# Kernel tuning notes

Measured on AMD Instinct MI355X. Metric: run time of the kernel, lower is better.

The kernel has to match this reference:

```python
import jax, jax.numpy as jnp
import numpy as np

V = 50257   # vocab_size
D = 128     # embed_dim
B = 1024    # batch of center words
C = 10      # context window size


def setup_inputs() -> dict:
    key = jax.random.key(0)
    ks = jax.random.split(key, 12)
    s = 0.05  # small init scale for linear weights
    return {
        "center_id": jax.random.randint(ks[0], (B,), 0, V),
        "context_ids": jax.random.randint(ks[1], (B, C), 0, V),
        "epsilon": jax.random.normal(ks[2], (D,), dtype=jnp.float32),
        # embedding tables init uniform(-1, 1) as in the torch module
        "emb": jax.random.uniform(ks[3], (V, D), minval=-1.0, maxval=1.0, dtype=jnp.float32),
        "prior_means": jax.random.uniform(ks[4], (V, D), minval=-1.0, maxval=1.0, dtype=jnp.float32),
        "prior_vars": jax.random.uniform(ks[5], (V, D), minval=-1.0, maxval=1.0, dtype=jnp.float32),
        "W_enc": jax.random.normal(ks[6], (2 * D, 2 * D), dtype=jnp.float32) * s,
        "b_enc": jnp.zeros((2 * D,), dtype=jnp.float32),
        "W_mean": jax.random.normal(ks[7], (2 * D, D), dtype=jnp.float32) * s,
        "b_mean": jnp.zeros((D,), dtype=jnp.float32),
        "W_var": jax.random.normal(ks[8], (2 * D, D), dtype=jnp.float32) * s,
        "b_var": jnp.zeros((D,), dtype=jnp.float32),
        "W_vocab": jax.random.normal(ks[9], (D, V), dtype=jnp.float32) * s,
        "b_vocab": jnp.zeros((V,), dtype=jnp.float32),
    }


def reference(center_id, context_ids, epsilon, emb, prior_means, prior_vars,
              W_enc, b_enc, W_mean, b_mean, W_var, b_var, W_vocab, b_vocab):
    ce = emb[center_id]                       # [B, D]
    cx = emb[context_ids]                     # [B, C, D]
    enc_in = jnp.concatenate(
        [jnp.broadcast_to(ce[:, None, :], cx.shape), cx], axis=-1)  # [B, C, 2D]
    h = jax.nn.relu(enc_in @ W_enc + b_enc).sum(axis=1)  # [B, 2D]
    mean = h @ W_mean + b_mean                           # [B, D]
    var = jax.nn.softplus(h @ W_var + b_var)             # [B, D] (diag cov s0)
    z = mean + jnp.exp(var / 2.0) * epsilon              # single shared epsilon [D]
    logits = z @ W_vocab + b_vocab                        # [B, V]
    logp = jax.nn.log_softmax(logits, axis=1)             # log(categorical)

    pm = prior_means[center_id]                           # m1 [B, D]
    pv = jax.nn.softplus(prior_vars[center_id])           # diag cov s1 [B, D]
    diff = pm - mean
    # closed-form diagonal Gaussian KL, identical math to the
    # trace/inverse/det formulation over diagflat matrices in the source
    kl = 0.5 * jnp.sum(var / pv + diff * diff / pv - 1.0
                       + jnp.log(pv) - jnp.log(var), axis=1)  # [B]

    # reconstruction: sum_k log categorical[i, context_ids[i, k]]
    rec = jnp.take_along_axis(logp, context_ids, axis=1).sum(axis=1)  # [B]

    return jnp.mean(rec - kl)
```

## Files before the change

### kernel.cpp

```cpp
#include <hip/hip_runtime.h>
#include <math.h>

#define VV 50257
#define VPAD 50304
#define DD 128
#define BB 1024
#define CC 10

typedef short bf16x8 __attribute__((ext_vector_type(8)));
typedef float f32x4 __attribute__((ext_vector_type(4)));

__device__ inline float bf2f(unsigned short u) {
    return __uint_as_float(((unsigned)u) << 16);
}
__device__ inline unsigned short f2bf(float f) {
    unsigned u = __float_as_uint(f);
    unsigned r = ((u >> 16) & 1) + 0x7FFF;
    return (unsigned short)((u + r) >> 16);
}


__global__ __launch_bounds__(256) void k_prep0(
    const float* __restrict__ W_enc, unsigned short* __restrict__ WeP)
{
    __shared__ float tl[256][17];
    const int jg = blockIdx.x, tid = threadIdx.x;
#pragma unroll
    for (int i = 0; i < 16; ++i) {
        int idx = i * 256 + tid;
        int k = idx >> 4, j = idx & 15;
        tl[k][j] = W_enc[(size_t)k * 256 + jg * 16 + j];
    }
    __syncthreads();
#pragma unroll
    for (int i = 0; i < 2; ++i) {
        int c = i * 256 + tid;
        int l15 = c & 15, q = (c >> 4) & 3, kI = c >> 6;
        bf16x8 o;
#pragma unroll
        for (int e = 0; e < 8; ++e)
            o[e] = (short)f2bf(tl[kI * 32 + q * 8 + e][l15]);
        *(bf16x8*)(WeP + (((size_t)jg * 8 + kI) * 64 + q * 16 + l15) * 8) = o;
    }
}

#define AS_STRIDE 520
__global__ __launch_bounds__(256) void k_main(
    const int* __restrict__ center_id, const int* __restrict__ context_ids,
    const float* __restrict__ emb, const unsigned short* __restrict__ WeP,
    const float* __restrict__ b_enc, const float* __restrict__ Wv,
    const float* __restrict__ W_mean, const float* __restrict__ W_var,
    unsigned short* __restrict__ WvP, unsigned short* __restrict__ Wmv,
    float* __restrict__ h)
{
    __shared__ __align__(16) unsigned char smraw[50688];
    const int bid = blockIdx.x, tid = threadIdx.x;

    if (bid >= 818) {
        const int b4 = bid - 818;
#pragma unroll
        for (int i = 0; i < 32; ++i) {
            int idx = b4 * 8192 + i * 256 + tid;
            unsigned short m = f2bf(W_mean[idx]);
            unsigned short v = f2bf(W_var[idx]);
            *(ushort2*)(Wmv + (size_t)idx * 2) = make_ushort2(m, v);
        }
        return;
    }

    if (bid >= 32) {
        float (*tile)[65] = (float (*)[65])smraw;
        const int s = bid - 32;
        const int v0 = s * 64;
#pragma unroll
        for (int i = 0; i < 32; ++i) {
            int idx = tid + i * 256;
            int k = idx >> 6, j = idx & 63;
            int v = v0 + j;
            tile[k][j] = (v < VV) ? Wv[(size_t)k * VV + v] : 0.f;
        }
        __syncthreads();
#pragma unroll
        for (int i = 0; i < 4; ++i) {
            int c = i * 256 + tid;
            int l15 = c & 15, q = (c >> 4) & 3, kI = (c >> 6) & 3, g = c >> 8;
            bf16x8 o;
#pragma unroll
            for (int e = 0; e < 8; ++e)
                o[e] = (short)f2bf(tile[kI * 32 + q * 8 + e][g * 16 + l15]);
            size_t vg = (size_t)s * 4 + g;
            *(bf16x8*)(WvP + ((vg * 4 + kI) * 64 + q * 16 + l15) * 8) = o;
        }
        return;
    }

    unsigned short* As = (unsigned short*)smraw;

    const int lane = tid & 63;
    const int wid  = tid >> 6;
    const int wm   = wid & 1;
    const int wn   = wid >> 1;
    const int quad = lane >> 4;
    const int l15  = lane & 15;

    const int bt = bid & 15;
    const int zt = bid >> 4;
    const int b0 = bt * 64;
    const int n0 = zt * 128;

    const int rlane = tid >> 4;
    const int c8    = tid & 15;
    const int kIc   = c8 >> 2, qc = c8 & 3;

#pragma unroll
    for (int p = 0; p < 4; ++p) {
        int r = p * 16 + rlane;
        int rid_ce = center_id[b0 + r];
        const float* s0 = emb + (size_t)rid_ce * 128 + c8 * 8;
        float4 a0 = *(const float4*)s0, a1 = *(const float4*)(s0 + 4);
        bf16x8 oa;
        oa[0] = (short)f2bf(a0.x); oa[1] = (short)f2bf(a0.y);
        oa[2] = (short)f2bf(a0.z); oa[3] = (short)f2bf(a0.w);
        oa[4] = (short)f2bf(a1.x); oa[5] = (short)f2bf(a1.y);
        oa[6] = (short)f2bf(a1.z); oa[7] = (short)f2bf(a1.w);
        *(bf16x8*)(As + (size_t)(p * 8 + kIc) * AS_STRIDE + (qc * 16 + rlane) * 8) = oa;
    }
#pragma unroll
    for (int p = 0; p < 4; ++p) {
        int r = p * 16 + rlane;
        int rid_cx = context_ids[(b0 + r) * CC + 0];
        const float* s1 = emb + (size_t)rid_cx * 128 + c8 * 8;
        float4 b0v = *(const float4*)s1, b1v = *(const float4*)(s1 + 4);
        bf16x8 ob;
        ob[0] = (short)f2bf(b0v.x); ob[1] = (short)f2bf(b0v.y);
        ob[2] = (short)f2bf(b0v.z); ob[3] = (short)f2bf(b0v.w);
        ob[4] = (short)f2bf(b1v.x); ob[5] = (short)f2bf(b1v.y);
        ob[6] = (short)f2bf(b1v.z); ob[7] = (short)f2bf(b1v.w);
        *(bf16x8*)(As + (size_t)(p * 8 + kIc + 4) * AS_STRIDE + (qc * 16 + rlane) * 8) = ob;
    }
    __syncthreads();

    float benc[4];
#pragma unroll
    for (int nt = 0; nt < 4; ++nt)
        benc[nt] = b_enc[n0 + wn * 64 + nt * 16 + l15];

    bf16x8 bbot[4][4];
#pragma unroll
    for (int nt = 0; nt < 4; ++nt) {
        size_t jg = (size_t)zt * 8 + wn * 4 + nt;
#pragma unroll
        for (int kI = 0; kI < 4; ++kI)
            bbot[nt][kI] = *(const bf16x8*)(WeP + ((jg * 8 + kI + 4) * 64 + lane) * 8);
    }

    f32x4 acc_ce[2][4];
#pragma unroll
    for (int mt = 0; mt < 2; ++mt)
#pragma unroll
        for (int nt = 0; nt < 4; ++nt) acc_ce[mt][nt] = (f32x4){0.f, 0.f, 0.f, 0.f};
#pragma unroll
    for (int kI = 0; kI < 4; ++kI) {
        bf16x8 a[2], b[4];
#pragma unroll
        for (int mt = 0; mt < 2; ++mt)
            a[mt] = *(const bf16x8*)(As + (size_t)((wm * 2 + mt) * 8 + kI) * AS_STRIDE + lane * 8);
#pragma unroll
        for (int nt = 0; nt < 4; ++nt) {
            size_t jg = (size_t)zt * 8 + wn * 4 + nt;
            b[nt] = *(const bf16x8*)(WeP + ((jg * 8 + kI) * 64 + lane) * 8);
        }
#pragma unroll
        for (int mt = 0; mt < 2; ++mt)
#pragma unroll
            for (int nt = 0; nt < 4; ++nt)
                acc_ce[mt][nt] = __builtin_amdgcn_mfma_f32_16x16x32_bf16(
                    a[mt], b[nt], acc_ce[mt][nt], 0, 0, 0);
    }

    float hacc[2][4][4];
#pragma unroll
    for (int mt = 0; mt < 2; ++mt)
#pragma unroll
        for (int nt = 0; nt < 4; ++nt)
#pragma unroll
            for (int reg = 0; reg < 4; ++reg) hacc[mt][nt][reg] = 0.f;

    for (int c = 0; c < CC; ++c) {
        f32x4 acc[2][4];
#pragma unroll
        for (int mt = 0; mt < 2; ++mt)
#pragma unroll
            for (int nt = 0; nt < 4; ++nt) acc[mt][nt] = acc_ce[mt][nt];
#pragma unroll
        for (int kI = 0; kI < 4; ++kI) {
            bf16x8 a[2];
#pragma unroll
            for (int mt = 0; mt < 2; ++mt)
                a[mt] = *(const bf16x8*)(As + (size_t)((wm * 2 + mt) * 8 + kI + 4) * AS_STRIDE + lane * 8);
#pragma unroll
            for (int mt = 0; mt < 2; ++mt)
#pragma unroll
                for (int nt = 0; nt < 4; ++nt)
                    acc[mt][nt] = __builtin_amdgcn_mfma_f32_16x16x32_bf16(
                        a[mt], bbot[nt][kI], acc[mt][nt], 0, 0, 0);
        }
#pragma unroll
        for (int mt = 0; mt < 2; ++mt)
#pragma unroll
            for (int nt = 0; nt < 4; ++nt)
#pragma unroll
                for (int reg = 0; reg < 4; ++reg)
                    hacc[mt][nt][reg] += fmaxf(acc[mt][nt][reg] + benc[nt], 0.f);

        if (c < CC - 1) {
            __syncthreads();
#pragma unroll
            for (int p = 0; p < 4; ++p) {
                int r = p * 16 + rlane;
                int rid_cx = context_ids[(b0 + r) * CC + (c + 1)];
                const float* s1 = emb + (size_t)rid_cx * 128 + c8 * 8;
                float4 b0v = *(const float4*)s1, b1v = *(const float4*)(s1 + 4);
                bf16x8 ob;
                ob[0] = (short)f2bf(b0v.x); ob[1] = (short)f2bf(b0v.y);
                ob[2] = (short)f2bf(b0v.z); ob[3] = (short)f2bf(b0v.w);
                ob[4] = (short)f2bf(b1v.x); ob[5] = (short)f2bf(b1v.y);
                ob[6] = (short)f2bf(b1v.z); ob[7] = (short)f2bf(b1v.w);
                *(bf16x8*)(As + (size_t)(p * 8 + kIc + 4) * AS_STRIDE + (qc * 16 + rlane) * 8) = ob;
            }
            __syncthreads();
        }
    }

    __syncthreads();
    float (*Csf)[132] = (float (*)[132])smraw;
#pragma unroll
    for (int mt = 0; mt < 2; ++mt)
#pragma unroll
        for (int nt = 0; nt < 4; ++nt) {
            int col = wn * 64 + nt * 16 + l15;
#pragma unroll
            for (int reg = 0; reg < 4; ++reg) {
                int row = wm * 32 + mt * 16 + quad * 4 + reg;
                Csf[row][col] = hacc[mt][nt][reg];
            }
        }
    __syncthreads();
#pragma unroll
    for (int it = 0; it < 8; ++it) {
        int ch = it * 256 + tid;
        int row = ch >> 5, cg = ch & 31;
        *(float4*)&h[(size_t)(b0 + row) * 256 + n0 + cg * 4] = *(const float4*)&Csf[row][cg * 4];
    }
}

__global__ __launch_bounds__(512) void k_latent(
    const float* __restrict__ h, const unsigned short* __restrict__ Wmv,
    const float* __restrict__ b_mean, const float* __restrict__ b_var,
    const float* __restrict__ epsilon,
    const int* __restrict__ center_id, const int* __restrict__ context_ids,
    const unsigned short* __restrict__ WvP, const float* __restrict__ bv,
    const float* __restrict__ prior_means, const float* __restrict__ prior_vars,
    unsigned short* __restrict__ z_pack, float* __restrict__ kl,
    float* __restrict__ ctxsum, float* __restrict__ out)
{
    __shared__ __align__(16) float hs[4][256];
    __shared__ float mpart[3][4][128], vpart[3][4][128];
    __shared__ float zsh[4][128];
    __shared__ float red[4][2];
    __shared__ float credw[4][2];
    const int tid = threadIdx.x;
    const int b0 = blockIdx.x * 4;

    if (blockIdx.x == 0 && tid == 0) out[0] = 0.f;

    {
        const int col = tid & 255;
        const int rr  = tid >> 8;
#pragma unroll
        for (int r2 = 0; r2 < 2; ++r2) {
            int row = rr * 2 + r2;
            hs[row][col] = h[(size_t)(b0 + row) * 256 + col];
        }
    }
    __syncthreads();

    const int d    = tid & 127;
    const int part = tid >> 7;
    const int kbase = part * 64;
    float m[4], vr[4];
#pragma unroll
    for (int r = 0; r < 4; ++r) {
        m[r]  = part ? 0.f : b_mean[d];
        vr[r] = part ? 0.f : b_var[d];
    }
    for (int k0 = 0; k0 < 64; k0 += 4) {
        float4 h4[4];
#pragma unroll
        for (int r = 0; r < 4; ++r)
            h4[r] = *(const float4*)&hs[r][kbase + k0];
#pragma unroll
        for (int kk = 0; kk < 4; ++kk) {
            ushort2 u = *(const ushort2*)(Wmv + ((size_t)(kbase + k0 + kk) * 128 + d) * 2);
            float wm_ = bf2f(u.x), wv_ = bf2f(u.y);
#pragma unroll
            for (int r = 0; r < 4; ++r) {
                float hk = ((const float*)&h4[r])[kk];
                m[r]  += hk * wm_;
                vr[r] += hk * wv_;
            }
        }
    }
    if (part) {
#pragma unroll
        for (int r = 0; r < 4; ++r) {
            mpart[part - 1][r][d] = m[r];
            vpart[part - 1][r][d] = vr[r];
        }
    }
    __syncthreads();

    if (tid < 128) {
        const int wid = tid >> 6;
        const int kIz = d >> 5, qz = (d >> 3) & 3, ez = d & 7;
        const int bg = b0 >> 4;
#pragma unroll
        for (int r = 0; r < 4; ++r) {
            float mm = m[r]  + mpart[0][r][d] + mpart[1][r][d] + mpart[2][r][d];
            float vv = vr[r] + vpart[0][r][d] + vpart[1][r][d] + vpart[2][r][d];

            float var = (vv > 20.f) ? vv : log1pf(__expf(vv));
            float zd = mm + __expf(0.5f * var) * epsilon[d];
            unsigned short zu = f2bf(zd);
            const int bb = b0 + r;
            const int l15b = bb & 15;
            z_pack[(((size_t)(bg * 4 + kIz)) * 64 + qz * 16 + l15b) * 8 + ez] = zu;
            zsh[r][d] = bf2f(zu);

            int cid = center_id[bb];
            float pm  = prior_means[(size_t)cid * 128 + d];
            float pvr = prior_vars[(size_t)cid * 128 + d];
            float pv  = (pvr > 20.f) ? pvr : log1pf(__expf(pvr));
            float diff = pm - mm;
            float t = var / pv + diff * diff / pv - 1.f + logf(pv) - logf(var);
#pragma unroll
            for (int off = 32; off; off >>= 1) t += __shfl_xor(t, off, 64);
            if ((tid & 63) == 0) red[r][wid] = t;
        }
    }
    __syncthreads();

    {
        const int w     = tid >> 6;
        const int row   = w & 3;
        const int phalf = w >> 2;
        const int lane  = tid & 63;
        const float z1 = zsh[row][lane];
        const float z2 = zsh[row][lane + 64];
        const int kI1 = lane >> 5, q1 = (lane >> 3) & 3, e1 = lane & 7;
        const int d2  = lane + 64;
        const int kI2 = d2 >> 5,  q2 = (d2 >> 3) & 3,  e2 = d2 & 7;
        float cacc = 0.f;
#pragma unroll
        for (int pp = 0; pp < 5; ++pp) {
            int p = phalf * 5 + pp;
            int cid = context_ids[(b0 + row) * CC + p];
            int vg = cid >> 4, l15v = cid & 15;
            float w1 = bf2f(WvP[(((size_t)(vg * 4 + kI1)) * 64 + q1 * 16 + l15v) * 8 + e1]);
            float w2 = bf2f(WvP[(((size_t)(vg * 4 + kI2)) * 64 + q2 * 16 + l15v) * 8 + e2]);
            float cs = z1 * w1 + z2 * w2;
#pragma unroll
            for (int off = 32; off; off >>= 1) cs += __shfl_xor(cs, off, 64);
            cacc += cs + bv[cid];
        }
        if (lane == 0) credw[row][phalf] = cacc;
    }
    __syncthreads();
    if (tid < 4) {
        kl[b0 + tid]     = 0.5f * (red[tid][0] + red[tid][1]);
        ctxsum[b0 + tid] = credw[tid][0] + credw[tid][1];
    }
}

__global__ __launch_bounds__(256) void k_lse(
    const unsigned short* __restrict__ z_pack, const unsigned short* __restrict__ WvP,
    const float* __restrict__ bv, float* __restrict__ partial)
{
    __shared__ float pl[2][128][20];
    const int x = blockIdx.x + 8 * blockIdx.y;
    if (x >= 393) return;
    const int mg = blockIdx.z;

    const int tid  = threadIdx.x;
    const int lane = tid & 63;
    const int wid  = tid >> 6;
    const int wm   = wid & 1;
    const int wn   = wid >> 1;
    const int quad = lane >> 4;
    const int l15  = lane & 15;
    const int n0   = x * 128;

    bf16x8 bfr[4][4];
#pragma unroll
    for (int nt = 0; nt < 4; ++nt) {
        size_t vg = (size_t)x * 8 + wn * 4 + nt;
#pragma unroll
        for (int kI = 0; kI < 4; ++kI)
            bfr[nt][kI] = *(const bf16x8*)(WvP + ((vg * 4 + kI) * 64 + lane) * 8);
    }

    float bvf[4];
#pragma unroll
    for (int nt = 0; nt < 4; ++nt) {
        int n = n0 + wn * 64 + nt * 16 + l15;
        bvf[nt] = (n < VV) ? bv[n] : -__builtin_huge_valf();
    }

#pragma unroll
    for (int mi = 0; mi < 4; ++mi) {
        const int mi_g = mg * 4 + mi;

        f32x4 acc[4][4];
#pragma unroll
        for (int mt = 0; mt < 4; ++mt)
#pragma unroll
            for (int nt = 0; nt < 4; ++nt) acc[mt][nt] = (f32x4){0.f, 0.f, 0.f, 0.f};

#pragma unroll
        for (int kI = 0; kI < 4; ++kI) {
            bf16x8 afr[4];
#pragma unroll
            for (int mt = 0; mt < 4; ++mt) {
                size_t bg = (size_t)mi_g * 8 + wm * 4 + mt;
                afr[mt] = *(const bf16x8*)(z_pack + ((bg * 4 + kI) * 64 + lane) * 8);
            }
#pragma unroll
            for (int mt = 0; mt < 4; ++mt)
#pragma unroll
                for (int nt = 0; nt < 4; ++nt)
                    acc[mt][nt] = __builtin_amdgcn_mfma_f32_16x16x32_bf16(
                        afr[mt], bfr[nt][kI], acc[mt][nt], 0, 0, 0);
        }

#pragma unroll
        for (int mt = 0; mt < 4; ++mt)
#pragma unroll
            for (int reg = 0; reg < 4; ++reg) {
                float s = 0.f;
#pragma unroll
                for (int nt = 0; nt < 4; ++nt)
                    s += __expf(acc[mt][nt][reg] + bvf[nt]);
                pl[wn][wm * 64 + mt * 16 + quad * 4 + reg][l15] = s;
            }
        __syncthreads();
        if (tid < 128) {
            const float* p0 = &pl[0][tid][0];
            const float* p1 = &pl[1][tid][0];
            float4 a0 = *(const float4*)(p0);
            float4 a1 = *(const float4*)(p0 + 4);
            float4 a2 = *(const float4*)(p0 + 8);
            float4 a3 = *(const float4*)(p0 + 12);
            float4 b0 = *(const float4*)(p1);
            float4 b1 = *(const float4*)(p1 + 4);
            float4 b2 = *(const float4*)(p1 + 8);
            float4 b3 = *(const float4*)(p1 + 12);
            float tot = (a0.x + a0.y + a0.z + a0.w) + (a1.x + a1.y + a1.z + a1.w)
                      + (a2.x + a2.y + a2.z + a2.w) + (a3.x + a3.y + a3.z + a3.w)
                      + (b0.x + b0.y + b0.z + b0.w) + (b1.x + b1.y + b1.z + b1.w)
                      + (b2.x + b2.y + b2.z + b2.w) + (b3.x + b3.y + b3.z + b3.w);
            partial[(size_t)x * 1024 + mi_g * 128 + tid] = tot;
        }
        __syncthreads();
    }
}

__global__ __launch_bounds__(256) void k_reduce(
    const float* __restrict__ partial, const float* __restrict__ ctxsum,
    const float* __restrict__ kl, float* __restrict__ out)
{
    __shared__ float bred[4];
    const int tid = threadIdx.x;
    const int row = blockIdx.x * 16 + (tid >> 4);
    const int part = tid & 15;

    float s = 0.f;
    for (int vb = part; vb < 393; vb += 16)
        s += partial[(size_t)vb * 1024 + row];
    s += __shfl_xor(s, 1, 64);
    s += __shfl_xor(s, 2, 64);
    s += __shfl_xor(s, 4, 64);
    s += __shfl_xor(s, 8, 64);

    float v = 0.f;
    if (part == 0)
        v = ctxsum[row] - 10.f * logf(s) - kl[row];
    v += __shfl_xor(v, 16, 64);
    v += __shfl_xor(v, 32, 64);
    if ((tid & 63) == 0) bred[tid >> 6] = v;
    __syncthreads();
    if (tid == 0)
        atomicAdd(out, (bred[0] + bred[1] + bred[2] + bred[3]) * (1.f / 1024.f));
}

extern "C" void kernel_launch(void* const* d_in, const int* in_sizes, int n_in,
                              void* d_out, int out_size, void* d_ws, size_t ws_size,
                              hipStream_t stream)
{
    const int*   center_id   = (const int*)d_in[0];
    const int*   context_ids = (const int*)d_in[1];
    const float* epsilon     = (const float*)d_in[2];
    const float* emb         = (const float*)d_in[3];
    const float* prior_means = (const float*)d_in[4];
    const float* prior_vars  = (const float*)d_in[5];
    const float* W_enc       = (const float*)d_in[6];
    const float* b_enc       = (const float*)d_in[7];
    const float* W_mean      = (const float*)d_in[8];
    const float* b_mean      = (const float*)d_in[9];
    const float* W_var       = (const float*)d_in[10];
    const float* b_var       = (const float*)d_in[11];
    const float* W_vocab     = (const float*)d_in[12];
    const float* b_vocab     = (const float*)d_in[13];

    float* out = (float*)d_out;
    char*  ws  = (char*)d_ws;

    size_t off = 0;
    unsigned short* WvP      = (unsigned short*)(ws + off); off += 12877824;
    unsigned short* WeP      = (unsigned short*)(ws + off); off += 131072;
    unsigned short* Wmv      = (unsigned short*)(ws + off); off += 131072;
    unsigned short* z_pack   = (unsigned short*)(ws + off); off += 262144;
    float*          h        = (float*)(ws + off);          off += 1048576;
    float*          kl       = (float*)(ws + off);          off += 4096;
    float*          ctxsum   = (float*)(ws + off);          off += 4096;
    float*          partial  = (float*)(ws + off);          off += 1609728;

    k_prep0<<<16, 256, 0, stream>>>(W_enc, WeP);
    k_main<<<822, 256, 0, stream>>>(center_id, context_ids, emb, WeP, b_enc,
                                    W_vocab, W_mean, W_var, WvP, Wmv, h);
    k_latent<<<256, 512, 0, stream>>>(h, Wmv, b_mean, b_var, epsilon,
                                      center_id, context_ids, WvP, b_vocab,
                                      prior_means, prior_vars, z_pack, kl,
                                      ctxsum, out);
    k_lse<<<dim3(8, 50, 2), 256, 0, stream>>>(z_pack, WvP, b_vocab, partial);
    k_reduce<<<64, 256, 0, stream>>>(partial, ctxsum, kl, out);
}
```

Before: 203.1 us.

## Double-buffer context embedding loads in encoder and split LSE grid finer

The encoder loop now prefetches the next context word's embedding rows into registers before the MFMA work and writes them into an alternating LDS buffer. This cuts one barrier per iteration and hides global gather latency behind compute. Separately, the log-sum-exp kernel processes half as many M-chunks per block and launches twice as many blocks along z, which raises parallelism. The trade-offs are higher register pressure from the prefetched data and more partial results for the reduce step to combine.

```diff
diff --git a/kernel.cpp b/kernel.cpp
--- a/kernel.cpp
+++ b/kernel.cpp
@@ -111,6 +111,7 @@
     const int rlane = tid >> 4;
     const int c8    = tid & 15;
     const int kIc   = c8 >> 2, qc = c8 & 3;
+    const int colB  = (qc * 16 + rlane) * 8;
 
 #pragma unroll
     for (int p = 0; p < 4; ++p) {
@@ -123,7 +124,7 @@
         oa[2] = (short)f2bf(a0.z); oa[3] = (short)f2bf(a0.w);
         oa[4] = (short)f2bf(a1.x); oa[5] = (short)f2bf(a1.y);
         oa[6] = (short)f2bf(a1.z); oa[7] = (short)f2bf(a1.w);
-        *(bf16x8*)(As + (size_t)(p * 8 + kIc) * AS_STRIDE + (qc * 16 + rlane) * 8) = oa;
+        *(bf16x8*)(As + (size_t)(p * 8 + kIc) * AS_STRIDE + colB) = oa;
     }
 #pragma unroll
     for (int p = 0; p < 4; ++p) {
@@ -136,8 +137,12 @@
         ob[2] = (short)f2bf(b0v.z); ob[3] = (short)f2bf(b0v.w);
         ob[4] = (short)f2bf(b1v.x); ob[5] = (short)f2bf(b1v.y);
         ob[6] = (short)f2bf(b1v.z); ob[7] = (short)f2bf(b1v.w);
-        *(bf16x8*)(As + (size_t)(p * 8 + kIc + 4) * AS_STRIDE + (qc * 16 + rlane) * 8) = ob;
-    }
+        *(bf16x8*)(As + (size_t)(p * 8 + kIc + 4) * AS_STRIDE + colB) = ob;
+    }
+    int cidn[4];
+#pragma unroll
+    for (int p = 0; p < 4; ++p)
+        cidn[p] = context_ids[(b0 + p * 16 + rlane) * CC + 1];
     __syncthreads();
 
     float benc[4];
@@ -187,6 +192,23 @@
             for (int reg = 0; reg < 4; ++reg) hacc[mt][nt][reg] = 0.f;
 
     for (int c = 0; c < CC; ++c) {
+        float4 ga[4], gb[4];
+        if (c < CC - 1) {
+#pragma unroll
+            for (int p = 0; p < 4; ++p) {
+                const float* s1 = emb + (size_t)cidn[p] * 128 + c8 * 8;
+                ga[p] = *(const float4*)s1;
+                gb[p] = *(const float4*)(s1 + 4);
+            }
+        }
+        int cidn2[4];
+        if (c < CC - 2) {
+#pragma unroll
+            for (int p = 0; p < 4; ++p)
+                cidn2[p] = context_ids[(b0 + p * 16 + rlane) * CC + c + 2];
+        }
+
+        const int rsel = c & 1;
         f32x4 acc[2][4];
 #pragma unroll
         for (int mt = 0; mt < 2; ++mt)
@@ -196,8 +218,11 @@
         for (int kI = 0; kI < 4; ++kI) {
             bf16x8 a[2];
 #pragma unroll
-            for (int mt = 0; mt < 2; ++mt)
-                a[mt] = *(const bf16x8*)(As + (size_t)((wm * 2 + mt) * 8 + kI + 4) * AS_STRIDE + lane * 8);
+            for (int mt = 0; mt < 2; ++mt) {
+                int pg = wm * 2 + mt;
+                int row = rsel ? (32 + pg * 4 + kI) : (pg * 8 + 4 + kI);
+                a[mt] = *(const bf16x8*)(As + (size_t)row * AS_STRIDE + lane * 8);
+            }
 #pragma unroll
             for (int mt = 0; mt < 2; ++mt)
 #pragma unroll
@@ -214,25 +239,23 @@
                     hacc[mt][nt][reg] += fmaxf(acc[mt][nt][reg] + benc[nt], 0.f);
 
         if (c < CC - 1) {
-            __syncthreads();
+            const int wsel = (c + 1) & 1;
 #pragma unroll
             for (int p = 0; p < 4; ++p) {
-                int r = p * 16 + rlane;
-                int rid_cx = context_ids[(b0 + r) * CC + (c + 1)];
-                const float* s1 = emb + (size_t)rid_cx * 128 + c8 * 8;
-                float4 b0v = *(const float4*)s1, b1v = *(const float4*)(s1 + 4);
                 bf16x8 ob;
-                ob[0] = (short)f2bf(b0v.x); ob[1] = (short)f2bf(b0v.y);
-                ob[2] = (short)f2bf(b0v.z); ob[3] = (short)f2bf(b0v.w);
-                ob[4] = (short)f2bf(b1v.x); ob[5] = (short)f2bf(b1v.y);
-                ob[6] = (short)f2bf(b1v.z); ob[7] = (short)f2bf(b1v.w);
-                *(bf16x8*)(As + (size_t)(p * 8 + kIc + 4) * AS_STRIDE + (qc * 16 + rlane) * 8) = ob;
-            }
-            __syncthreads();
-        }
-    }
-
-    __syncthreads();
+                ob[0] = (short)f2bf(ga[p].x); ob[1] = (short)f2bf(ga[p].y);
+                ob[2] = (short)f2bf(ga[p].z); ob[3] = (short)f2bf(ga[p].w);
+                ob[4] = (short)f2bf(gb[p].x); ob[5] = (short)f2bf(gb[p].y);
+                ob[6] = (short)f2bf(gb[p].z); ob[7] = (short)f2bf(gb[p].w);
+                int row = wsel ? (32 + p * 4 + kIc) : (p * 8 + 4 + kIc);
+                *(bf16x8*)(As + (size_t)row * AS_STRIDE + colB) = ob;
+            }
+#pragma unroll
+            for (int p = 0; p < 4; ++p) cidn[p] = cidn2[p];
+        }
+        __syncthreads();
+    }
+
     float (*Csf)[132] = (float (*)[132])smraw;
 #pragma unroll
     for (int mt = 0; mt < 2; ++mt)
@@ -417,8 +440,8 @@
     }
 
 #pragma unroll
-    for (int mi = 0; mi < 4; ++mi) {
-        const int mi_g = mg * 4 + mi;
+    for (int mi = 0; mi < 2; ++mi) {
+        const int mi_g = mg * 2 + mi;
 
         f32x4 acc[4][4];
 #pragma unroll
@@ -541,6 +564,6 @@
                                       center_id, context_ids, WvP, b_vocab,
                                       prior_means, prior_vars, z_pack, kl,
                                       ctxsum, out);
-    k_lse<<<dim3(8, 50, 2), 256, 0, stream>>>(z_pack, WvP, b_vocab, partial);
+    k_lse<<<dim3(8, 50, 4), 256, 0, stream>>>(z_pack, WvP, b_vocab, partial);
     k_reduce<<<64, 256, 0, stream>>>(partial, ctxsum, kl, out);
 }
```

Result: no change. 199.5 us (-1.8%).
